# Kernel tuning notes

Hardware: AMD Instinct MI355X
Metric: run time of the kernel (lower is better)

The kernel has to match this reference:

```python
import jax, jax.numpy as jnp
import numpy as np

OPACITY_FACTOR = 0.8  # module-level global `opacity_factor` in the original repo


def setup_inputs() -> dict:
    key = jax.random.key(0)
    N, H, W = 128, 512, 512
    # Pre-rendered RGBA polygons (stand-in for Polygon(...)(h, w, param2img)),
    # values in [0,1]; channel 3 is alpha.
    polys = jax.random.uniform(key, (N, 1, 4, H, W), dtype=jnp.float32)
    return {"polys": polys, "h": H, "w": W}


def reference(polys, h, w):
    # canvas = ones((1,4,h,w)); sequentially alpha-composite each polygon:
    # canvas = canvas*(1 - alpha*op) + alpha*op*poly, alpha = poly[:,3:]
    canvas0 = jnp.ones((1, 4, h, w), dtype=polys.dtype)

    def step(canvas, poly):  # poly: (1,4,h,w)
        a = poly[:, 3:] * OPACITY_FACTOR  # (1,1,h,w), broadcasts over RGBA
        return canvas * (1.0 - a) + a * poly, None

    canvas, _ = jax.lax.scan(step, canvas0, polys)
    return canvas
```

## Files before the change

### kernel.cpp

```cpp
#include <hip/hip_runtime.h>


#define PH 512
#define PW 512
#define PHW (PH * PW)
#define PHW4 (PHW / 4)
#define OPACITY 0.8f

__device__ __forceinline__ void composite(float4& c, const float4& p, const float4& a) {
    c.x = fmaf(a.x, p.x - c.x, c.x);
    c.y = fmaf(a.y, p.y - c.y, c.y);
    c.z = fmaf(a.z, p.z - c.z, c.z);
    c.w = fmaf(a.w, p.w - c.w, c.w);
}

__global__ __launch_bounds__(256) void paint_kernel(const float4* __restrict__ polys,
                                                    float4* __restrict__ out,
                                                    int n_polys) {
    const int idx = blockIdx.x * blockDim.x + threadIdx.x;
    if (idx >= PHW4) return;

    const float4 one = make_float4(1.f, 1.f, 1.f, 1.f);
    float4 c0 = one, c1 = one, c2 = one, c3 = one;

    const float4* p = polys + idx;
    #pragma unroll 4
    for (int n = 0; n < n_polys; ++n) {
        const float4 p0 = p[0 * PHW4];
        const float4 p1 = p[1 * PHW4];
        const float4 p2 = p[2 * PHW4];
        const float4 p3 = p[3 * PHW4];
        p += 4 * PHW4;

        const float4 a = make_float4(p3.x * OPACITY, p3.y * OPACITY,
                                     p3.z * OPACITY, p3.w * OPACITY);
        composite(c0, p0, a);
        composite(c1, p1, a);
        composite(c2, p2, a);
        composite(c3, p3, a);
    }

    out[0 * PHW4 + idx] = c0;
    out[1 * PHW4 + idx] = c1;
    out[2 * PHW4 + idx] = c2;
    out[3 * PHW4 + idx] = c3;
}

extern "C" void kernel_launch(void* const* d_in, const int* in_sizes, int n_in,
                              void* d_out, int out_size, void* d_ws, size_t ws_size,
                              hipStream_t stream) {
    const float* polys = (const float*)d_in[0];
    float* out = (float*)d_out;

    const int n_polys = in_sizes[0] / (4 * PHW);

    const int threads = 256;
    const int blocks = (PHW4 + threads - 1) / threads;
    paint_kernel<<<blocks, threads, 0, stream>>>((const float4*)polys,
                                                 (float4*)out, n_polys);
}
```

Measured before the change: 663.4 us.

## Split polygon sequence into chunks and combine via associative affine compositing

Rewrites the sequential over-composite as an associative scan. Each chunk of polygons is reduced per pixel to a multiplicative transmittance plus an additive color term, stored in workspace, and a second kernel folds the chunk results in order. The goal is to launch about 16x more blocks than the single-pass kernel, which uses only one block per CU and is latency-bound on memory reads. The cost is extra workspace write and read traffic and a second launch. It falls back to the original kernel when workspace is missing or too small.

```diff
diff --git a/kernel.cpp b/kernel.cpp
--- a/kernel.cpp
+++ b/kernel.cpp
@@ -12,6 +12,67 @@
     c.y = fmaf(a.y, p.y - c.y, c.y);
     c.z = fmaf(a.z, p.z - c.z, c.z);
     c.w = fmaf(a.w, p.w - c.w, c.w);
+}
+
+__global__ __launch_bounds__(256) void paint_chunk(const float4* __restrict__ polys,
+                                                   float4* __restrict__ ws,
+                                                   int n_polys, int n_chunks) {
+    const int idx = blockIdx.x * blockDim.x + threadIdx.x;
+    const int chunk = blockIdx.y;
+    const int n0 = (int)(((long long)chunk * n_polys) / n_chunks);
+    const int n1 = (int)(((long long)(chunk + 1) * n_polys) / n_chunks);
+
+    float4 m = make_float4(1.f, 1.f, 1.f, 1.f);
+    float4 b0 = make_float4(0.f, 0.f, 0.f, 0.f);
+    float4 b1 = b0, b2 = b0, b3 = b0;
+
+    const float4* p = polys + (size_t)n0 * 4 * PHW4 + idx;
+    #pragma unroll 4
+    for (int n = n0; n < n1; ++n) {
+        const float4 p0 = p[0 * PHW4];
+        const float4 p1 = p[1 * PHW4];
+        const float4 p2 = p[2 * PHW4];
+        const float4 p3 = p[3 * PHW4];
+        p += 4 * PHW4;
+
+        const float4 a = make_float4(p3.x * OPACITY, p3.y * OPACITY,
+                                     p3.z * OPACITY, p3.w * OPACITY);
+        composite(b0, p0, a);
+        composite(b1, p1, a);
+        composite(b2, p2, a);
+        composite(b3, p3, a);
+        m.x *= 1.f - a.x;
+        m.y *= 1.f - a.y;
+        m.z *= 1.f - a.z;
+        m.w *= 1.f - a.w;
+    }
+
+    float4* w = ws + (size_t)chunk * 5 * PHW4 + idx;
+    w[0 * PHW4] = m;
+    w[1 * PHW4] = b0;
+    w[2 * PHW4] = b1;
+    w[3 * PHW4] = b2;
+    w[4 * PHW4] = b3;
+}
+
+__global__ __launch_bounds__(256) void combine_chunks(const float4* __restrict__ ws,
+                                                      float4* __restrict__ out,
+                                                      int n_chunks) {
+    const int idx = blockIdx.x * blockDim.x + threadIdx.x;
+    const int ch = blockIdx.y;
+    float4 c = make_float4(1.f, 1.f, 1.f, 1.f);
+    const float4* w = ws + idx;
+    #pragma unroll 4
+    for (int k = 0; k < n_chunks; ++k) {
+        const float4 mm = w[0 * PHW4];
+        const float4 bb = w[(1 + ch) * PHW4];
+        c.x = fmaf(mm.x, c.x, bb.x);
+        c.y = fmaf(mm.y, c.y, bb.y);
+        c.z = fmaf(mm.z, c.z, bb.z);
+        c.w = fmaf(mm.w, c.w, bb.w);
+        w += 5 * PHW4;
+    }
+    out[(size_t)ch * PHW4 + idx] = c;
 }
 
 __global__ __launch_bounds__(256) void paint_kernel(const float4* __restrict__ polys,
@@ -54,8 +115,25 @@
 
     const int n_polys = in_sizes[0] / (4 * PHW);
 
+    const size_t bytes_per_chunk = (size_t)5 * PHW4 * sizeof(float4);
+
+    int n_chunks = 16;
+    while (n_chunks > 1 && n_chunks > n_polys) n_chunks >>= 1;
+    while (n_chunks > 1 && (size_t)n_chunks * bytes_per_chunk > ws_size) n_chunks >>= 1;
+
     const int threads = 256;
-    const int blocks = (PHW4 + threads - 1) / threads;
-    paint_kernel<<<blocks, threads, 0, stream>>>((const float4*)polys,
-                                                 (float4*)out, n_polys);
+    if (d_ws == nullptr || n_chunks < 2 ||
+        (size_t)n_chunks * bytes_per_chunk > ws_size) {
+        const int blocks = (PHW4 + threads - 1) / threads;
+        paint_kernel<<<blocks, threads, 0, stream>>>((const float4*)polys,
+                                                     (float4*)out, n_polys);
+        return;
+    }
+
+    float4* ws = (float4*)d_ws;
+    dim3 g1(PHW4 / threads, n_chunks);
+    paint_chunk<<<g1, threads, 0, stream>>>((const float4*)polys, ws,
+                                            n_polys, n_chunks);
+    dim3 g2(PHW4 / threads, 4);
+    combine_chunks<<<g2, threads, 0, stream>>>(ws, (float4*)out, n_chunks);
 }
```

Result: slower. 701.5 us (+5.7%).

## Split polygon sequence into chunks composed as affine maps via parallel scan

Applied to the files above, without the earlier changes.

Each block now covers 64 pixel groups, and its 8 wavefronts each process a contiguous slice of the polygon sequence. Every wave builds an affine map (multiplier m and offset b) for its slice. The partial maps are written to LDS and composed in order to produce the final canvas. This parallelises the serial dependence over polygons so many more memory requests are in flight, which targets latency-bound streaming. The cost is extra FMAs for the multiplier, LDS traffic, and a block-wide barrier.

```diff
diff --git a/kernel.cpp b/kernel.cpp
--- a/kernel.cpp
+++ b/kernel.cpp
@@ -6,44 +6,86 @@
 #define PHW (PH * PW)
 #define PHW4 (PHW / 4)
 #define OPACITY 0.8f
+#define NCHUNK 8
 
-__device__ __forceinline__ void composite(float4& c, const float4& p, const float4& a) {
-    c.x = fmaf(a.x, p.x - c.x, c.x);
-    c.y = fmaf(a.y, p.y - c.y, c.y);
-    c.z = fmaf(a.z, p.z - c.z, c.z);
-    c.w = fmaf(a.w, p.w - c.w, c.w);
-}
+__global__ __launch_bounds__(512) void paint_scan(const float4* __restrict__ polys,
+                                                  float4* __restrict__ out,
+                                                  int n_polys) {
+    const int tid = threadIdx.x;
+    const int w   = tid >> 6;
+    const int l   = tid & 63;
+    const int group = blockIdx.x * 64 + l;
 
-__global__ __launch_bounds__(256) void paint_kernel(const float4* __restrict__ polys,
-                                                    float4* __restrict__ out,
-                                                    int n_polys) {
-    const int idx = blockIdx.x * blockDim.x + threadIdx.x;
-    if (idx >= PHW4) return;
+    const int n0 = (w * n_polys) / NCHUNK;
+    const int n1 = ((w + 1) * n_polys) / NCHUNK;
 
-    const float4 one = make_float4(1.f, 1.f, 1.f, 1.f);
-    float4 c0 = one, c1 = one, c2 = one, c3 = one;
+    float4 m  = make_float4(1.f, 1.f, 1.f, 1.f);
+    float4 b0 = make_float4(0.f, 0.f, 0.f, 0.f);
+    float4 b1 = b0, b2 = b0, b3 = b0;
 
-    const float4* p = polys + idx;
-    #pragma unroll 4
-    for (int n = 0; n < n_polys; ++n) {
+    const float4* p = polys + (size_t)n0 * 4 * PHW4 + group;
+    #pragma unroll 2
+    for (int n = n0; n < n1; ++n) {
         const float4 p0 = p[0 * PHW4];
         const float4 p1 = p[1 * PHW4];
         const float4 p2 = p[2 * PHW4];
         const float4 p3 = p[3 * PHW4];
         p += 4 * PHW4;
 
-        const float4 a = make_float4(p3.x * OPACITY, p3.y * OPACITY,
-                                     p3.z * OPACITY, p3.w * OPACITY);
-        composite(c0, p0, a);
-        composite(c1, p1, a);
-        composite(c2, p2, a);
-        composite(c3, p3, a);
+        const float ax = p3.x * OPACITY;
+        const float ay = p3.y * OPACITY;
+        const float az = p3.z * OPACITY;
+        const float aw = p3.w * OPACITY;
+
+        b0.x = fmaf(ax, p0.x - b0.x, b0.x);
+        b0.y = fmaf(ay, p0.y - b0.y, b0.y);
+        b0.z = fmaf(az, p0.z - b0.z, b0.z);
+        b0.w = fmaf(aw, p0.w - b0.w, b0.w);
+
+        b1.x = fmaf(ax, p1.x - b1.x, b1.x);
+        b1.y = fmaf(ay, p1.y - b1.y, b1.y);
+        b1.z = fmaf(az, p1.z - b1.z, b1.z);
+        b1.w = fmaf(aw, p1.w - b1.w, b1.w);
+
+        b2.x = fmaf(ax, p2.x - b2.x, b2.x);
+        b2.y = fmaf(ay, p2.y - b2.y, b2.y);
+        b2.z = fmaf(az, p2.z - b2.z, b2.z);
+        b2.w = fmaf(aw, p2.w - b2.w, b2.w);
+
+        b3.x = fmaf(ax, p3.x - b3.x, b3.x);
+        b3.y = fmaf(ay, p3.y - b3.y, b3.y);
+        b3.z = fmaf(az, p3.z - b3.z, b3.z);
+        b3.w = fmaf(aw, p3.w - b3.w, b3.w);
+
+        m.x = fmaf(-ax, m.x, m.x);
+        m.y = fmaf(-ay, m.y, m.y);
+        m.z = fmaf(-az, m.z, m.z);
+        m.w = fmaf(-aw, m.w, m.w);
     }
 
-    out[0 * PHW4 + idx] = c0;
-    out[1 * PHW4 + idx] = c1;
-    out[2 * PHW4 + idx] = c2;
-    out[3 * PHW4 + idx] = c3;
+    __shared__ float4 lds[NCHUNK][5][64];
+    lds[w][0][l] = m;
+    lds[w][1][l] = b0;
+    lds[w][2][l] = b1;
+    lds[w][3][l] = b2;
+    lds[w][4][l] = b3;
+    __syncthreads();
+
+    if (tid < 256) {
+        const int g  = tid & 63;
+        const int ch = tid >> 6;
+        float4 c = make_float4(1.f, 1.f, 1.f, 1.f);
+        #pragma unroll
+        for (int k = 0; k < NCHUNK; ++k) {
+            const float4 mm = lds[k][0][g];
+            const float4 bb = lds[k][1 + ch][g];
+            c.x = fmaf(mm.x, c.x, bb.x);
+            c.y = fmaf(mm.y, c.y, bb.y);
+            c.z = fmaf(mm.z, c.z, bb.z);
+            c.w = fmaf(mm.w, c.w, bb.w);
+        }
+        out[(size_t)ch * PHW4 + blockIdx.x * 64 + g] = c;
+    }
 }
 
 extern "C" void kernel_launch(void* const* d_in, const int* in_sizes, int n_in,
@@ -54,8 +96,8 @@
 
     const int n_polys = in_sizes[0] / (4 * PHW);
 
-    const int threads = 256;
-    const int blocks = (PHW4 + threads - 1) / threads;
-    paint_kernel<<<blocks, threads, 0, stream>>>((const float4*)polys,
-                                                 (float4*)out, n_polys);
+    const int threads = 512;
+    const int blocks = PHW4 / 64;
+    paint_scan<<<blocks, threads, 0, stream>>>((const float4*)polys,
+                                               (float4*)out, n_polys);
 }
```

Measured after the change: 689.2 us. 1.04x slower.
